# Optimization experiments

Hardware: AMD Instinct MI355X
Metric: run time of the kernel (lower is better)

The kernel has to match this reference:

```python
import jax, jax.numpy as jnp
import numpy as np
import math

N_HEAD = 16
N_KV_HEAD = 4
HEAD_DIM = 128  # n_embed // n_head


def apply_rope(x, omega, offset=0):
    # x: (B, T, H, D); omega: (D//2,) Llama-style inverse frequencies
    T = x.shape[1]
    d2 = x.shape[-1] // 2
    pos = (jnp.arange(T) + offset).astype(x.dtype)
    ang = pos[:, None] * omega[None, :]              # (T, d2)
    cos = jnp.cos(ang)[None, :, None, :]
    sin = jnp.sin(ang)[None, :, None, :]
    x1, x2 = x[..., :d2], x[..., d2:]
    return jnp.concatenate([x1 * cos - x2 * sin, x1 * sin + x2 * cos], axis=-1)


def setup_inputs() -> dict:
    key = jax.random.key(0)
    k1, k2, k3, k4 = jax.random.split(key, 4)
    B, T, C = 2, 2048, 2048
    std = 0.02
    x = jax.random.normal(k1, (B, T, C), dtype=jnp.float32)
    wq = jax.random.normal(k2, (C, C), dtype=jnp.float32) * std
    wkv = jax.random.normal(k3, (C, 2 * N_KV_HEAD * HEAD_DIM), dtype=jnp.float32) * std
    wproj = jax.random.normal(k4, (C, C), dtype=jnp.float32) * std * (2 * 24) ** (-0.5)
    # Llama RoPE frequencies: 1 / 10000^(2i/D)
    omega = (1.0 / (10000.0 ** (jnp.arange(0, HEAD_DIM, 2, dtype=jnp.float32) / HEAD_DIM)))
    return {"x": x, "wq": wq, "wkv": wkv, "wproj": wproj, "omega": omega}


def reference(x, wq, wkv, wproj, omega):
    B, T, C = x.shape
    H, KH, D = N_HEAD, N_KV_HEAD, HEAD_DIM
    G = H // KH  # query heads per kv head

    q = (x @ wq).reshape(B, T, H, D)
    kv = x @ wkv
    k, v = jnp.split(kv, 2, axis=-1)

    q = apply_rope(q, omega, offset=0)
    k = apply_rope(k.reshape(B, T, KH, D), omega, offset=0)
    v = v.reshape(B, T, KH, D)

    # GQA causal attention (no KV expansion: group query heads per kv head)
    qr = q.reshape(B, T, KH, G, D)
    scores = jnp.einsum('bqkgd,bskd->bkgqs', qr, k) / math.sqrt(D)
    causal = jnp.tril(jnp.ones((T, T), dtype=bool))
    scores = jnp.where(causal[None, None, None, :, :], scores, -jnp.inf)
    att = jax.nn.softmax(scores, axis=-1)
    y = jnp.einsum('bkgqs,bskd->bqkgd', att, v).reshape(B, T, C)
    return y @ wproj
```

## Files before the change

### kernel.cpp

```cpp
#include <hip/hip_runtime.h>
#include <hip/hip_bf16.h>

#define B_ 2
#define T_ 2048
#define C_ 2048
#define H_ 16
#define KH_ 4
#define D_ 128

typedef unsigned short ushort_t;
typedef __attribute__((ext_vector_type(8))) short short8;
typedef __attribute__((ext_vector_type(4))) float f32x4;

#define RSQRT_D 0.08838834764831845f
#define L2E 1.4426950408889634f

__device__ __forceinline__ ushort_t f2b(float f) {
  union { float f; unsigned u; } v; v.f = f;
  unsigned r = v.u + 0x7fffu + ((v.u >> 16) & 1u);
  return (ushort_t)(r >> 16);
}
__device__ __forceinline__ float b2f(ushort_t u) {
  union { unsigned u; float f; } v; v.u = ((unsigned)u) << 16;
  return v.f;
}

__device__ __forceinline__ f32x4 mfma16(short8 a, short8 b, f32x4 c) {
  return __builtin_amdgcn_mfma_f32_16x16x32_bf16(a, b, c, 0, 0, 0);
}

__device__ __forceinline__ void async16(const void* g, void* l) {
  __builtin_amdgcn_global_load_lds(
      (const __attribute__((address_space(1))) void*)g,
      (__attribute__((address_space(3))) void*)l, 16, 0, 0);
}

__device__ __forceinline__ unsigned cvtpk(float lo, float hi) {
  unsigned r;
  asm volatile("v_cvt_pk_bf16_f32 %0, %1, %2" : "=v"(r) : "v"(lo), "v"(hi));
  return r;
}


__global__ void convert_f32_bf16(const float* __restrict__ in, ushort_t* __restrict__ out, int n4) {
  int i = blockIdx.x * blockDim.x + threadIdx.x;
  if (i >= n4) return;
  float4 v = ((const float4*)in)[i];
  ushort4 o;
  o.x = f2b(v.x); o.y = f2b(v.y); o.z = f2b(v.z); o.w = f2b(v.w);
  ((ushort4*)out)[i] = o;
}

__global__ void transpose_to_bf16(const float* __restrict__ in, ushort_t* __restrict__ out, int R, int C) {
  __shared__ float tile[32][33];
  int c0 = blockIdx.x * 32, r0 = blockIdx.y * 32;
  int tx = threadIdx.x, ty = threadIdx.y;
#pragma unroll
  for (int i = 0; i < 4; i++) {
    int r = ty + i * 8;
    tile[r][tx] = in[(size_t)(r0 + r) * C + c0 + tx];
  }
  __syncthreads();
#pragma unroll
  for (int i = 0; i < 4; i++) {
    int r = ty + i * 8;
    out[(size_t)(c0 + r) * R + r0 + tx] = f2b(tile[tx][r]);
  }
}

__global__ void rope_tab_k(const float* __restrict__ omega, float2* __restrict__ tab) {
  int idx = blockIdx.x * blockDim.x + threadIdx.x;
  int d = idx & 63;
  int t = idx >> 6;
  float ang = (float)t * omega[d];
  tab[idx] = make_float2(cosf(ang), sinf(ang));
}

__global__ void rope_q_k(const ushort_t* __restrict__ QKVraw, const float2* __restrict__ tab,
                         ushort_t* __restrict__ Qb) {
  int idx = blockIdx.x * blockDim.x + threadIdx.x;
  int d = idx & 63;
  int h = (idx >> 6) & 15;
  int t = (idx >> 10) & 2047;
  int b = idx >> 21;
  size_t in_off = (size_t)(b * 2048 + t) * 3072 + h * 128 + d;
  float x1 = b2f(QKVraw[in_off]);
  float x2 = b2f(QKVraw[in_off + 64]);
  float2 cs = tab[t * 64 + d];
  size_t out_off = ((size_t)(b * 16 + h) * 2048 + t) * 128 + d;
  Qb[out_off] = f2b((x1 * cs.x - x2 * cs.y) * RSQRT_D);
  Qb[out_off + 64] = f2b((x1 * cs.y + x2 * cs.x) * RSQRT_D);
}

__global__ void rope_k_k(const ushort_t* __restrict__ QKVraw, const float2* __restrict__ tab,
                         ushort_t* __restrict__ Kb) {
  int idx = blockIdx.x * blockDim.x + threadIdx.x;
  int d = idx & 63;
  int kh = (idx >> 6) & 3;
  int t = (idx >> 8) & 2047;
  int b = idx >> 19;
  size_t in_off = (size_t)(b * 2048 + t) * 3072 + 2048 + kh * 128 + d;
  float x1 = b2f(QKVraw[in_off]);
  float x2 = b2f(QKVraw[in_off + 64]);
  float2 cs = tab[t * 64 + d];
  size_t out_off = ((size_t)(b * 4 + kh) * 2048 + t) * 128 + d;
  Kb[out_off] = f2b(x1 * cs.x - x2 * cs.y);
  Kb[out_off + 64] = f2b(x1 * cs.y + x2 * cs.x);
}

__global__ void v_frag_k(const ushort_t* __restrict__ QKVraw, ushort_t* __restrict__ Vf) {
  int idx = blockIdx.x * blockDim.x + threadIdx.x;
  int lane = idx & 63;
  int n = (idx >> 6) & 7;
  int hv = (idx >> 9) & 1;
  int tile = (idx >> 10) & 31;
  int z = idx >> 15;
  int b = z >> 2, kh = z & 3;
  int lr = lane & 15, lc = lane >> 4;
  int d = n * 16 + lr;
  union { ushort_t u[8]; short8 v; } out;
#pragma unroll
  for (int j = 0; j < 8; j++) {
    int tw = j >> 1, par = j & 1;
    int kl = (hv * 2 + (tw >> 1)) * 16 + lc * 4 + 2 * (tw & 1) + par;
    int t = tile * 64 + kl;
    out.u[j] = QKVraw[(size_t)(b * 2048 + t) * 3072 + 2560 + kh * 128 + d];
  }
  *(short8*)(Vf + (size_t)idx * 8) = out.v;
}


__device__ __forceinline__ void store_out(float* C, size_t idx, float v) { C[idx] = v; }
__device__ __forceinline__ void store_out(ushort_t* C, size_t idx, float v) { C[idx] = f2b(v); }

template <typename OUT_T>
__global__ __launch_bounds__(256) void gemm_bt(const ushort_t* __restrict__ A,
                                               const ushort_t* __restrict__ Bt,
                                               OUT_T* __restrict__ C,
                                               int M, int N, int K) {
  __shared__ __attribute__((aligned(16))) ushort_t As[2][128 * 32];
  __shared__ __attribute__((aligned(16))) ushort_t Bs[2][128 * 32];
  const int tid = threadIdx.x;
  const int lane = tid & 63;
  const int w = tid >> 6;
  const int bm = blockIdx.y, bn = blockIdx.x;
  const int lr = lane & 15, lc = lane >> 4;
  const int wr = (w >> 1) * 64, wc = (w & 1) * 64;
  const ushort_t* Ab = A + (size_t)bm * 128 * K;
  const ushort_t* Bb = Bt + (size_t)bn * 128 * K;
  const int srow = tid >> 2;
  const int scol = (tid & 3) * 8;
  f32x4 acc[4][4];
#pragma unroll
  for (int i = 0; i < 4; i++)
#pragma unroll
    for (int j = 0; j < 4; j++) acc[i][j] = (f32x4)(0.0f);

  {
    async16(Ab + (size_t)srow * K + scol, &As[0][0] + srow * 32 + scol);
    async16(Ab + (size_t)(srow + 64) * K + scol, &As[0][0] + (srow + 64) * 32 + scol);
    async16(Bb + (size_t)srow * K + scol, &Bs[0][0] + srow * 32 + scol);
    async16(Bb + (size_t)(srow + 64) * K + scol, &Bs[0][0] + (srow + 64) * 32 + scol);
  }
  __syncthreads();

  const int nt = K >> 5;
#pragma unroll 2
  for (int t = 0; t < nt; t++) {
    const int cur = t & 1;
    if (t + 1 < nt) {
      const int k1 = (t + 1) << 5;
      ushort_t* Ad = &As[cur ^ 1][0];
      ushort_t* Bd = &Bs[cur ^ 1][0];
      async16(Ab + (size_t)srow * K + k1 + scol, Ad + srow * 32 + scol);
      async16(Ab + (size_t)(srow + 64) * K + k1 + scol, Ad + (srow + 64) * 32 + scol);
      async16(Bb + (size_t)srow * K + k1 + scol, Bd + srow * 32 + scol);
      async16(Bb + (size_t)(srow + 64) * K + k1 + scol, Bd + (srow + 64) * 32 + scol);
    }
    const ushort_t* Al = &As[cur][0];
    const ushort_t* Bl = &Bs[cur][0];
    short8 af[4], bf[4];
#pragma unroll
    for (int mi = 0; mi < 4; mi++)
      af[mi] = *(const short8*)(Al + (wr + mi * 16 + lr) * 32 + lc * 8);
#pragma unroll
    for (int ni = 0; ni < 4; ni++)
      bf[ni] = *(const short8*)(Bl + (wc + ni * 16 + lr) * 32 + lc * 8);
#pragma unroll
    for (int mi = 0; mi < 4; mi++)
#pragma unroll
      for (int ni = 0; ni < 4; ni++)
        acc[mi][ni] = mfma16(af[mi], bf[ni], acc[mi][ni]);
    __syncthreads();
  }
#pragma unroll
  for (int mi = 0; mi < 4; mi++) {
#pragma unroll
    for (int ni = 0; ni < 4; ni++) {
      int row = bm * 128 + wr + mi * 16 + lc * 4;
      int col = bn * 128 + wc + ni * 16 + lr;
#pragma unroll
      for (int r = 0; r < 4; r++)
        store_out(C, (size_t)(row + r) * N + col, acc[mi][ni][r]);
    }
  }
}

__global__ __launch_bounds__(256, 2) void attn_k(const ushort_t* __restrict__ Qb,
                                                 const ushort_t* __restrict__ Kb,
                                                 const ushort_t* __restrict__ Vf,
                                                 ushort_t* __restrict__ Yb) {
  __shared__ __attribute__((aligned(16))) ushort_t Ks[2][64 * 128];
  const int tid = threadIdx.x;
  const int lane = tid & 63;
  const int w = tid >> 6;
  const int lr = lane & 15, lc = lane >> 4;
  const int h = blockIdx.y;
  const int b = blockIdx.z;
  const int kh = h >> 2;
  const int bx = blockIdx.x;

  const ushort_t* Qp = Qb + (size_t)(b * 16 + h) * T_ * D_;
  const ushort_t* Kp = Kb + (size_t)(b * 4 + kh) * T_ * D_;
  const ushort_t* Vfb = Vf + (size_t)(b * 4 + kh) * 262144;

  const int st_row = tid >> 4;
  const int st_slot = tid & 15;

#pragma unroll 1
  for (int pass = 0; pass < 2; pass++) {
    const int qc = pass ? (31 - bx) : bx;
    const int q0w = qc * 64 + w * 16;
    const int q = q0w + lr;

    short8 qf[4];
#pragma unroll
    for (int c = 0; c < 4; c++)
      qf[c] = *(const short8*)(Qp + (size_t)(q0w + lr) * D_ + c * 32 + lc * 8);

    f32x4 o[8];
#pragma unroll
    for (int n = 0; n < 8; n++) o[n] = (f32x4)(0.0f);
    float m = -1e30f, l = 0.0f;

    const int nt = qc + 1;

    __syncthreads();
#pragma unroll
    for (int i = 0; i < 4; i++) {
      int row = i * 16 + st_row;
      async16(Kp + (size_t)row * D_ + (((st_slot - row) & 15) * 8),
              &Ks[0][0] + row * 128 + st_slot * 8);
    }

#pragma unroll 1
    for (int ti = 0; ti < nt; ti++) {
      __syncthreads();
      const int kv0 = ti * 64;
      if (ti + 1 < nt) {
        const ushort_t* Kn = Kp + (size_t)(kv0 + 64) * D_;
        ushort_t* dst = &Ks[(ti + 1) & 1][0];
#pragma unroll
        for (int i = 0; i < 4; i++) {
          int row = i * 16 + st_row;
          async16(Kn + (size_t)row * D_ + (((st_slot - row) & 15) * 8),
                  dst + row * 128 + st_slot * 8);
        }
      }
      const ushort_t* Kl = &Ks[ti & 1][0];
      const ushort_t* Vt0 = Vfb + (size_t)(ti * 2) * 4096;
      short8 vr0[8];
#pragma unroll
      for (int n = 0; n < 8; n++)
        vr0[n] = *(const short8*)(Vt0 + n * 512 + lane * 8);
      f32x4 s[4];
#pragma unroll
      for (int kj = 0; kj < 4; kj++) s[kj] = (f32x4)(0.0f);
      __builtin_amdgcn_s_setprio(1);
#pragma unroll
      for (int c = 0; c < 4; c++) {
        short8 kf[4];
#pragma unroll
        for (int kj = 0; kj < 4; kj++)
          kf[kj] = *(const short8*)(Kl + (kj * 16 + lr) * 128 + (((c * 4 + lc + lr) & 15) * 8));
#pragma unroll
        for (int kj = 0; kj < 4; kj++)
          s[kj] = mfma16(kf[kj], qf[c], s[kj]);
      }
      __builtin_amdgcn_s_setprio(0);
      const ushort_t* Vt1 = Vfb + (size_t)(ti * 2 + 1) * 4096;
      short8 vr1[8];
#pragma unroll
      for (int n = 0; n < 8; n++)
        vr1[n] = *(const short8*)(Vt1 + n * 512 + lane * 8);
      float pv[16];
      float mx = -1e30f;
      if (kv0 + 63 > q0w) {
#pragma unroll
        for (int kj = 0; kj < 4; kj++)
#pragma unroll
          for (int r = 0; r < 4; r++) {
            float a = s[kj][r];
            if (kv0 + kj * 16 + lc * 4 + r > q) a = -1e30f;
            pv[kj * 4 + r] = a;
            mx = fmaxf(mx, a);
          }
      } else {
#pragma unroll
        for (int kj = 0; kj < 4; kj++)
#pragma unroll
          for (int r = 0; r < 4; r++) {
            float a = s[kj][r];
            pv[kj * 4 + r] = a;
            mx = fmaxf(mx, a);
          }
      }
      mx = fmaxf(mx, __shfl_xor(mx, 16));
      mx = fmaxf(mx, __shfl_xor(mx, 32));
      const bool need = __any(mx > m + 5.5f);
      const float mn = need ? fmaxf(m, mx) : m;
      float rs = 0.0f;
#pragma unroll
      for (int i = 0; i < 16; i++) {
        pv[i] = exp2f((pv[i] - mn) * L2E);
        rs += pv[i];
      }
      rs += __shfl_xor(rs, 16);
      rs += __shfl_xor(rs, 32);
      unsigned Wd[8];
#pragma unroll
      for (int kj = 0; kj < 4; kj++) {
        Wd[kj * 2] = cvtpk(pv[kj * 4], pv[kj * 4 + 1]);
        Wd[kj * 2 + 1] = cvtpk(pv[kj * 4 + 2], pv[kj * 4 + 3]);
      }
      union { unsigned u[4]; short8 v; } pa0, pa1;
#pragma unroll
      for (int t = 0; t < 4; t++) { pa0.u[t] = Wd[t]; pa1.u[t] = Wd[4 + t]; }
      if (need) {
        float al = exp2f((m - mn) * L2E);
        m = mn;
        l = l * al + rs;
        float alT[4];
#pragma unroll
        for (int r = 0; r < 4; r++)
          alT[r] = __shfl(al, (lane & 48) | (lc * 4 + r));
#pragma unroll
        for (int n = 0; n < 8; n++)
#pragma unroll
          for (int r = 0; r < 4; r++) o[n][r] *= alT[r];
      } else {
        l += rs;
      }
      __builtin_amdgcn_s_setprio(1);
#pragma unroll
      for (int n = 0; n < 8; n++) o[n] = mfma16(pa0.v, vr0[n], o[n]);
#pragma unroll
      for (int n = 0; n < 8; n++) o[n] = mfma16(pa1.v, vr1[n], o[n]);
      __builtin_amdgcn_s_setprio(0);
    }
    float inv = 1.0f / l;
    float invT[4];
#pragma unroll
    for (int r = 0; r < 4; r++)
      invT[r] = __shfl(inv, (lane & 48) | (lc * 4 + r));
#pragma unroll
    for (int n = 0; n < 8; n++)
#pragma unroll
      for (int r = 0; r < 4; r++) {
        int qo = q0w + lc * 4 + r;
        int d = n * 16 + lr;
        Yb[(size_t)(b * T_ + qo) * 2048 + h * 128 + d] = f2b(o[n][r] * invT[r]);
      }
  }
}


extern "C" void kernel_launch(void* const* d_in, const int* in_sizes, int n_in,
                              void* d_out, int out_size, void* d_ws, size_t ws_size,
                              hipStream_t stream) {
  (void)in_sizes; (void)n_in; (void)out_size; (void)ws_size;
  const float* x = (const float*)d_in[0];
  const float* wq = (const float*)d_in[1];
  const float* wkv = (const float*)d_in[2];
  const float* wproj = (const float*)d_in[3];
  const float* omega = (const float*)d_in[4];
  float* out = (float*)d_out;
  char* ws = (char*)d_ws;

  ushort_t* xb     = (ushort_t*)(ws + 0);
  ushort_t* wqkvT  = (ushort_t*)(ws + 16777216);
  ushort_t* wkvT   = (ushort_t*)(ws + 25165824);
  ushort_t* wprojT = (ushort_t*)(ws + 29360128);
  ushort_t* QKVraw = (ushort_t*)(ws + 37748736);
  ushort_t* Qb     = (ushort_t*)(ws + 62914560);
  ushort_t* Kb     = (ushort_t*)(ws + 79691776);
  ushort_t* Vf     = (ushort_t*)(ws + 83886080);
  ushort_t* Yb     = (ushort_t*)(ws + 88080384);
  float2*   tab    = (float2*)(ws + 104857600);

  convert_f32_bf16<<<8192, 256, 0, stream>>>(x, xb, 2097152);
  transpose_to_bf16<<<dim3(64, 64), dim3(32, 8), 0, stream>>>(wq, wqkvT, 2048, 2048);
  transpose_to_bf16<<<dim3(32, 64), dim3(32, 8), 0, stream>>>(wkv, wkvT, 2048, 1024);
  transpose_to_bf16<<<dim3(64, 64), dim3(32, 8), 0, stream>>>(wproj, wprojT, 2048, 2048);
  rope_tab_k<<<512, 256, 0, stream>>>(omega, tab);

  gemm_bt<<<dim3(24, 32), 256, 0, stream>>>(xb, wqkvT, QKVraw, 4096, 3072, 2048);

  rope_q_k<<<16384, 256, 0, stream>>>(QKVraw, tab, Qb);
  rope_k_k<<<4096, 256, 0, stream>>>(QKVraw, tab, Kb);
  v_frag_k<<<1024, 256, 0, stream>>>(QKVraw, Vf);

  attn_k<<<dim3(16, 16, 2), 256, 0, stream>>>(Qb, Kb, Vf, Yb);

  gemm_bt<<<dim3(16, 32), 256, 0, stream>>>(Yb, wprojT, out, 4096, 2048, 2048);
}
```

Baseline: 222.6 us.

## Split attention into one query chunk per block, fold log2e into Q, pipeline GEMM waits

The attention kernel stops pairing a short and a long causal query chunk in one block. It launches one block per query chunk, heaviest chunks first, and raises the occupancy hint to 4 blocks per CU. The log2(e) factor is folded into the Q scaling so the softmax skips a multiply per element, and the rescale threshold changes from 5.5 to 8. The GEMM main loop replaces __syncthreads with an explicit vmcnt wait plus raw barriers and peels the last iteration, aiming to overlap loads better. Risks include load imbalance from uneven block lengths and tighter register pressure at 4 blocks per CU.

```diff
diff --git a/kernel.cpp b/kernel.cpp
--- a/kernel.cpp
+++ b/kernel.cpp
@@ -14,6 +14,7 @@
 
 #define RSQRT_D 0.08838834764831845f
 #define L2E 1.4426950408889634f
+#define QSCALE (0.08838834764831845f * 1.4426950408889634f)
 
 __device__ __forceinline__ ushort_t f2b(float f) {
   union { float f; unsigned u; } v; v.f = f;
@@ -88,8 +89,8 @@
   float x2 = b2f(QKVraw[in_off + 64]);
   float2 cs = tab[t * 64 + d];
   size_t out_off = ((size_t)(b * 16 + h) * 2048 + t) * 128 + d;
-  Qb[out_off] = f2b((x1 * cs.x - x2 * cs.y) * RSQRT_D);
-  Qb[out_off + 64] = f2b((x1 * cs.y + x2 * cs.x) * RSQRT_D);
+  Qb[out_off] = f2b((x1 * cs.x - x2 * cs.y) * QSCALE);
+  Qb[out_off + 64] = f2b((x1 * cs.y + x2 * cs.x) * QSCALE);
 }
 
 __global__ void rope_k_k(const ushort_t* __restrict__ QKVraw, const float2* __restrict__ tab,
@@ -156,19 +157,16 @@
 #pragma unroll
     for (int j = 0; j < 4; j++) acc[i][j] = (f32x4)(0.0f);
 
-  {
-    async16(Ab + (size_t)srow * K + scol, &As[0][0] + srow * 32 + scol);
-    async16(Ab + (size_t)(srow + 64) * K + scol, &As[0][0] + (srow + 64) * 32 + scol);
-    async16(Bb + (size_t)srow * K + scol, &Bs[0][0] + srow * 32 + scol);
-    async16(Bb + (size_t)(srow + 64) * K + scol, &Bs[0][0] + (srow + 64) * 32 + scol);
-  }
-  __syncthreads();
+  async16(Ab + (size_t)srow * K + scol, &As[0][0] + srow * 32 + scol);
+  async16(Ab + (size_t)(srow + 64) * K + scol, &As[0][0] + (srow + 64) * 32 + scol);
+  async16(Bb + (size_t)srow * K + scol, &Bs[0][0] + srow * 32 + scol);
+  async16(Bb + (size_t)(srow + 64) * K + scol, &Bs[0][0] + (srow + 64) * 32 + scol);
 
   const int nt = K >> 5;
 #pragma unroll 2
-  for (int t = 0; t < nt; t++) {
+  for (int t = 0; t < nt - 1; t++) {
     const int cur = t & 1;
-    if (t + 1 < nt) {
+    {
       const int k1 = (t + 1) << 5;
       ushort_t* Ad = &As[cur ^ 1][0];
       ushort_t* Bd = &Bs[cur ^ 1][0];
@@ -177,6 +175,9 @@
       async16(Bb + (size_t)srow * K + k1 + scol, Bd + srow * 32 + scol);
       async16(Bb + (size_t)(srow + 64) * K + k1 + scol, Bd + (srow + 64) * 32 + scol);
     }
+    asm volatile("s_waitcnt vmcnt(4)" ::: "memory");
+    __builtin_amdgcn_s_barrier();
+    __builtin_amdgcn_sched_barrier(0);
     const ushort_t* Al = &As[cur][0];
     const ushort_t* Bl = &Bs[cur][0];
     short8 af[4], bf[4];
@@ -191,7 +192,29 @@
 #pragma unroll
       for (int ni = 0; ni < 4; ni++)
         acc[mi][ni] = mfma16(af[mi], bf[ni], acc[mi][ni]);
-    __syncthreads();
+    asm volatile("" ::: "memory");
+    __builtin_amdgcn_s_barrier();
+    asm volatile("" ::: "memory");
+  }
+  {
+    const int cur = (nt - 1) & 1;
+    asm volatile("s_waitcnt vmcnt(0)" ::: "memory");
+    __builtin_amdgcn_s_barrier();
+    __builtin_amdgcn_sched_barrier(0);
+    const ushort_t* Al = &As[cur][0];
+    const ushort_t* Bl = &Bs[cur][0];
+    short8 af[4], bf[4];
+#pragma unroll
+    for (int mi = 0; mi < 4; mi++)
+      af[mi] = *(const short8*)(Al + (wr + mi * 16 + lr) * 32 + lc * 8);
+#pragma unroll
+    for (int ni = 0; ni < 4; ni++)
+      bf[ni] = *(const short8*)(Bl + (wc + ni * 16 + lr) * 32 + lc * 8);
+#pragma unroll
+    for (int mi = 0; mi < 4; mi++)
+#pragma unroll
+      for (int ni = 0; ni < 4; ni++)
+        acc[mi][ni] = mfma16(af[mi], bf[ni], acc[mi][ni]);
   }
 #pragma unroll
   for (int mi = 0; mi < 4; mi++) {
@@ -206,7 +229,7 @@
   }
 }
 
-__global__ __launch_bounds__(256, 2) void attn_k(const ushort_t* __restrict__ Qb,
+__global__ __launch_bounds__(256, 4) void attn_k(const ushort_t* __restrict__ Qb,
                                                  const ushort_t* __restrict__ Kb,
                                                  const ushort_t* __restrict__ Vf,
                                                  ushort_t* __restrict__ Yb) {
@@ -218,7 +241,9 @@
   const int h = blockIdx.y;
   const int b = blockIdx.z;
   const int kh = h >> 2;
-  const int bx = blockIdx.x;
+  const int qc = 31 - blockIdx.x;
+  const int q0w = qc * 64 + w * 16;
+  const int q = q0w + lr;
 
   const ushort_t* Qp = Qb + (size_t)(b * 16 + h) * T_ * D_;
   const ushort_t* Kp = Kb + (size_t)(b * 4 + kh) * T_ * D_;
@@ -227,151 +252,143 @@
   const int st_row = tid >> 4;
   const int st_slot = tid & 15;
 
+  short8 qf[4];
+#pragma unroll
+  for (int c = 0; c < 4; c++)
+    qf[c] = *(const short8*)(Qp + (size_t)(q0w + lr) * D_ + c * 32 + lc * 8);
+
+  f32x4 o[8];
+#pragma unroll
+  for (int n = 0; n < 8; n++) o[n] = (f32x4)(0.0f);
+  float m = -1e30f, l = 0.0f;
+
+  const int nt = qc + 1;
+
+#pragma unroll
+  for (int i = 0; i < 4; i++) {
+    int row = i * 16 + st_row;
+    async16(Kp + (size_t)row * D_ + (((st_slot - row) & 15) * 8),
+            &Ks[0][0] + row * 128 + st_slot * 8);
+  }
+
 #pragma unroll 1
-  for (int pass = 0; pass < 2; pass++) {
-    const int qc = pass ? (31 - bx) : bx;
-    const int q0w = qc * 64 + w * 16;
-    const int q = q0w + lr;
-
-    short8 qf[4];
-#pragma unroll
-    for (int c = 0; c < 4; c++)
-      qf[c] = *(const short8*)(Qp + (size_t)(q0w + lr) * D_ + c * 32 + lc * 8);
-
-    f32x4 o[8];
-#pragma unroll
-    for (int n = 0; n < 8; n++) o[n] = (f32x4)(0.0f);
-    float m = -1e30f, l = 0.0f;
-
-    const int nt = qc + 1;
-
+  for (int ti = 0; ti < nt; ti++) {
     __syncthreads();
-#pragma unroll
-    for (int i = 0; i < 4; i++) {
-      int row = i * 16 + st_row;
-      async16(Kp + (size_t)row * D_ + (((st_slot - row) & 15) * 8),
-              &Ks[0][0] + row * 128 + st_slot * 8);
-    }
-
-#pragma unroll 1
-    for (int ti = 0; ti < nt; ti++) {
-      __syncthreads();
-      const int kv0 = ti * 64;
-      if (ti + 1 < nt) {
-        const ushort_t* Kn = Kp + (size_t)(kv0 + 64) * D_;
-        ushort_t* dst = &Ks[(ti + 1) & 1][0];
-#pragma unroll
-        for (int i = 0; i < 4; i++) {
-          int row = i * 16 + st_row;
-          async16(Kn + (size_t)row * D_ + (((st_slot - row) & 15) * 8),
-                  dst + row * 128 + st_slot * 8);
+    const int kv0 = ti * 64;
+    if (ti + 1 < nt) {
+      const ushort_t* Kn = Kp + (size_t)(kv0 + 64) * D_;
+      ushort_t* dst = &Ks[(ti + 1) & 1][0];
+#pragma unroll
+      for (int i = 0; i < 4; i++) {
+        int row = i * 16 + st_row;
+        async16(Kn + (size_t)row * D_ + (((st_slot - row) & 15) * 8),
+                dst + row * 128 + st_slot * 8);
+      }
+    }
+    const ushort_t* Kl = &Ks[ti & 1][0];
+    const ushort_t* Vt0 = Vfb + (size_t)(ti * 2) * 4096;
+    short8 vr0[8];
+#pragma unroll
+    for (int n = 0; n < 8; n++)
+      vr0[n] = *(const short8*)(Vt0 + n * 512 + lane * 8);
+    f32x4 s[4];
+#pragma unroll
+    for (int kj = 0; kj < 4; kj++) s[kj] = (f32x4)(0.0f);
+    __builtin_amdgcn_s_setprio(1);
+#pragma unroll
+    for (int c = 0; c < 4; c++) {
+      short8 kf[4];
+#pragma unroll
+      for (int kj = 0; kj < 4; kj++)
+        kf[kj] = *(const short8*)(Kl + (kj * 16 + lr) * 128 + (((c * 4 + lc + lr) & 15) * 8));
+#pragma unroll
+      for (int kj = 0; kj < 4; kj++)
+        s[kj] = mfma16(kf[kj], qf[c], s[kj]);
+    }
+    __builtin_amdgcn_s_setprio(0);
+    const ushort_t* Vt1 = Vfb + (size_t)(ti * 2 + 1) * 4096;
+    short8 vr1[8];
+#pragma unroll
+    for (int n = 0; n < 8; n++)
+      vr1[n] = *(const short8*)(Vt1 + n * 512 + lane * 8);
+    float pv[16];
+    float mx = -1e30f;
+    if (kv0 + 63 > q0w) {
+#pragma unroll
+      for (int kj = 0; kj < 4; kj++)
+#pragma unroll
+        for (int r = 0; r < 4; r++) {
+          float a = s[kj][r];
+          if (kv0 + kj * 16 + lc * 4 + r > q) a = -1e30f;
+          pv[kj * 4 + r] = a;
+          mx = fmaxf(mx, a);
         }
-      }
-      const ushort_t* Kl = &Ks[ti & 1][0];
-      const ushort_t* Vt0 = Vfb + (size_t)(ti * 2) * 4096;
-      short8 vr0[8];
+    } else {
+#pragma unroll
+      for (int kj = 0; kj < 4; kj++)
+#pragma unroll
+        for (int r = 0; r < 4; r++) {
+          float a = s[kj][r];
+          pv[kj * 4 + r] = a;
+          mx = fmaxf(mx, a);
+        }
+    }
+    mx = fmaxf(mx, __shfl_xor(mx, 16));
+    mx = fmaxf(mx, __shfl_xor(mx, 32));
+    const bool need = __any(mx > m + 8.0f);
+    const float mn = need ? fmaxf(m, mx) : m;
+    float rs = 0.0f;
+#pragma unroll
+    for (int i = 0; i < 16; i++) {
+      pv[i] = exp2f(pv[i] - mn);
+      rs += pv[i];
+    }
+    rs += __shfl_xor(rs, 16);
+    rs += __shfl_xor(rs, 32);
+    unsigned Wd[8];
+#pragma unroll
+    for (int kj = 0; kj < 4; kj++) {
+      Wd[kj * 2] = cvtpk(pv[kj * 4], pv[kj * 4 + 1]);
+      Wd[kj * 2 + 1] = cvtpk(pv[kj * 4 + 2], pv[kj * 4 + 3]);
+    }
+    union { unsigned u[4]; short8 v; } pa0, pa1;
+#pragma unroll
+    for (int t = 0; t < 4; t++) { pa0.u[t] = Wd[t]; pa1.u[t] = Wd[4 + t]; }
+    if (need) {
+      float al = exp2f(m - mn);
+      m = mn;
+      l = l * al + rs;
+      float alT[4];
+#pragma unroll
+      for (int r = 0; r < 4; r++)
+        alT[r] = __shfl(al, (lane & 48) | (lc * 4 + r));
 #pragma unroll
       for (int n = 0; n < 8; n++)
-        vr0[n] = *(const short8*)(Vt0 + n * 512 + lane * 8);
-      f32x4 s[4];
-#pragma unroll
-      for (int kj = 0; kj < 4; kj++) s[kj] = (f32x4)(0.0f);
-      __builtin_amdgcn_s_setprio(1);
-#pragma unroll
-      for (int c = 0; c < 4; c++) {
-        short8 kf[4];
-#pragma unroll
-        for (int kj = 0; kj < 4; kj++)
-          kf[kj] = *(const short8*)(Kl + (kj * 16 + lr) * 128 + (((c * 4 + lc + lr) & 15) * 8));
-#pragma unroll
-        for (int kj = 0; kj < 4; kj++)
-          s[kj] = mfma16(kf[kj], qf[c], s[kj]);
-      }
-      __builtin_amdgcn_s_setprio(0);
-      const ushort_t* Vt1 = Vfb + (size_t)(ti * 2 + 1) * 4096;
-      short8 vr1[8];
-#pragma unroll
-      for (int n = 0; n < 8; n++)
-        vr1[n] = *(const short8*)(Vt1 + n * 512 + lane * 8);
-      float pv[16];
-      float mx = -1e30f;
-      if (kv0 + 63 > q0w) {
-#pragma unroll
-        for (int kj = 0; kj < 4; kj++)
-#pragma unroll
-          for (int r = 0; r < 4; r++) {
-            float a = s[kj][r];
-            if (kv0 + kj * 16 + lc * 4 + r > q) a = -1e30f;
-            pv[kj * 4 + r] = a;
-            mx = fmaxf(mx, a);
-          }
-      } else {
-#pragma unroll
-        for (int kj = 0; kj < 4; kj++)
-#pragma unroll
-          for (int r = 0; r < 4; r++) {
-            float a = s[kj][r];
-            pv[kj * 4 + r] = a;
-            mx = fmaxf(mx, a);
-          }
-      }
-      mx = fmaxf(mx, __shfl_xor(mx, 16));
-      mx = fmaxf(mx, __shfl_xor(mx, 32));
-      const bool need = __any(mx > m + 5.5f);
-      const float mn = need ? fmaxf(m, mx) : m;
-      float rs = 0.0f;
-#pragma unroll
-      for (int i = 0; i < 16; i++) {
-        pv[i] = exp2f((pv[i] - mn) * L2E);
-        rs += pv[i];
-      }
-      rs += __shfl_xor(rs, 16);
-      rs += __shfl_xor(rs, 32);
-      unsigned Wd[8];
-#pragma unroll
-      for (int kj = 0; kj < 4; kj++) {
-        Wd[kj * 2] = cvtpk(pv[kj * 4], pv[kj * 4 + 1]);
-        Wd[kj * 2 + 1] = cvtpk(pv[kj * 4 + 2], pv[kj * 4 + 3]);
-      }
-      union { unsigned u[4]; short8 v; } pa0, pa1;
-#pragma unroll
-      for (int t = 0; t < 4; t++) { pa0.u[t] = Wd[t]; pa1.u[t] = Wd[4 + t]; }
-      if (need) {
-        float al = exp2f((m - mn) * L2E);
-        m = mn;
-        l = l * al + rs;
-        float alT[4];
-#pragma unroll
-        for (int r = 0; r < 4; r++)
-          alT[r] = __shfl(al, (lane & 48) | (lc * 4 + r));
-#pragma unroll
-        for (int n = 0; n < 8; n++)
-#pragma unroll
-          for (int r = 0; r < 4; r++) o[n][r] *= alT[r];
-      } else {
-        l += rs;
-      }
-      __builtin_amdgcn_s_setprio(1);
-#pragma unroll
-      for (int n = 0; n < 8; n++) o[n] = mfma16(pa0.v, vr0[n], o[n]);
-#pragma unroll
-      for (int n = 0; n < 8; n++) o[n] = mfma16(pa1.v, vr1[n], o[n]);
-      __builtin_amdgcn_s_setprio(0);
-    }
-    float inv = 1.0f / l;
-    float invT[4];
-#pragma unroll
-    for (int r = 0; r < 4; r++)
-      invT[r] = __shfl(inv, (lane & 48) | (lc * 4 + r));
-#pragma unroll
-    for (int n = 0; n < 8; n++)
-#pragma unroll
-      for (int r = 0; r < 4; r++) {
-        int qo = q0w + lc * 4 + r;
-        int d = n * 16 + lr;
-        Yb[(size_t)(b * T_ + qo) * 2048 + h * 128 + d] = f2b(o[n][r] * invT[r]);
-      }
-  }
+#pragma unroll
+        for (int r = 0; r < 4; r++) o[n][r] *= alT[r];
+    } else {
+      l += rs;
+    }
+    __builtin_amdgcn_s_setprio(1);
+#pragma unroll
+    for (int n = 0; n < 8; n++) o[n] = mfma16(pa0.v, vr0[n], o[n]);
+#pragma unroll
+    for (int n = 0; n < 8; n++) o[n] = mfma16(pa1.v, vr1[n], o[n]);
+    __builtin_amdgcn_s_setprio(0);
+  }
+  float inv = 1.0f / l;
+  float invT[4];
+#pragma unroll
+  for (int r = 0; r < 4; r++)
+    invT[r] = __shfl(inv, (lane & 48) | (lc * 4 + r));
+#pragma unroll
+  for (int n = 0; n < 8; n++)
+#pragma unroll
+    for (int r = 0; r < 4; r++) {
+      int qo = q0w + lc * 4 + r;
+      int d = n * 16 + lr;
+      Yb[(size_t)(b * T_ + qo) * 2048 + h * 128 + d] = f2b(o[n][r] * invT[r]);
+    }
 }
 
 
@@ -410,7 +427,7 @@
   rope_k_k<<<4096, 256, 0, stream>>>(QKVraw, tab, Kb);
   v_frag_k<<<1024, 256, 0, stream>>>(QKVraw, Vf);
 
-  attn_k<<<dim3(16, 16, 2), 256, 0, stream>>>(Qb, Kb, Vf, Yb);
+  attn_k<<<dim3(32, 16, 2), 256, 0, stream>>>(Qb, Kb, Vf, Yb);
 
   gemm_bt<<<dim3(16, 32), 256, 0, stream>>>(Yb, wprojT, out, 4096, 2048, 2048);
 }
```

Measured after the change: 454.0 us. 2.04x slower.
